# Kernel tuning notes

Hardware: AMD Instinct MI355X
Metric: run time of the kernel (lower is better)

Reference implementation:

```python
import jax, jax.numpy as jnp
import numpy as np

H = W = 9
C = 16
D = 34
NHEAD = 2
HDIM = D // NHEAD  # 17
FF = 2048
NLAYERS = 2
EPS = 1e-5


def setup_inputs() -> dict:
    key = jax.random.key(0)
    ks = jax.random.split(key, 16)
    s = 0.05
    return {
        "obs": jax.random.normal(ks[0], (2, H, W), dtype=jnp.float32),
        "conv1_w": jax.random.normal(ks[1], (16, 2, 3, 3), dtype=jnp.float32) * s,
        "conv1_b": jnp.zeros((16,), jnp.float32),
        "conv2_w": jax.random.normal(ks[2], (16, 16, 3, 3), dtype=jnp.float32) * s,
        "conv2_b": jnp.zeros((16,), jnp.float32),
        "in_proj_w": jax.random.normal(ks[3], (NLAYERS, 3 * D, D), dtype=jnp.float32) * s,
        "in_proj_b": jnp.zeros((NLAYERS, 3 * D), jnp.float32),
        "out_proj_w": jax.random.normal(ks[4], (NLAYERS, D, D), dtype=jnp.float32) * s,
        "out_proj_b": jnp.zeros((NLAYERS, D), jnp.float32),
        "lin1_w": jax.random.normal(ks[5], (NLAYERS, FF, D), dtype=jnp.float32) * s,
        "lin1_b": jnp.zeros((NLAYERS, FF), jnp.float32),
        "lin2_w": jax.random.normal(ks[6], (NLAYERS, D, FF), dtype=jnp.float32) * s,
        "lin2_b": jnp.zeros((NLAYERS, D), jnp.float32),
        "ln1_g": jnp.ones((NLAYERS, D), jnp.float32),
        "ln1_b": jnp.zeros((NLAYERS, D), jnp.float32),
        "ln2_g": jnp.ones((NLAYERS, D), jnp.float32),
        "ln2_b": jnp.zeros((NLAYERS, D), jnp.float32),
    }


def _layer_norm(x, g, b):
    m = jnp.mean(x, axis=-1, keepdims=True)
    v = jnp.mean(jnp.square(x - m), axis=-1, keepdims=True)
    return (x - m) * jax.lax.rsqrt(v + EPS) * g + b


def _encoder_layer(x, ipw, ipb, opw, opb, l1w, l1b, l2w, l2b, g1, b1, g2, b2):
    # x: [S, D]. Post-norm TransformerEncoderLayer, eval mode (no dropout).
    S = x.shape[0]
    qkv = x @ ipw.T + ipb  # [S, 3D]
    q, k, v = jnp.split(qkv, 3, axis=-1)
    q = q.reshape(S, NHEAD, HDIM).transpose(1, 0, 2)  # [h, S, d]
    k = k.reshape(S, NHEAD, HDIM).transpose(1, 0, 2)
    v = v.reshape(S, NHEAD, HDIM).transpose(1, 0, 2)
    scores = jnp.einsum("hqd,hkd->hqk", q, k) / jnp.sqrt(jnp.float32(HDIM))
    attn = jax.nn.softmax(scores, axis=-1)
    o = jnp.einsum("hqk,hkd->hqd", attn, v)  # [h, S, d]
    o = o.transpose(1, 0, 2).reshape(S, D)
    o = o @ opw.T + opb
    x = _layer_norm(x + o, g1, b1)
    f = jax.nn.relu(x @ l1w.T + l1b) @ l2w.T + l2b
    return _layer_norm(x + f, g2, b2)


def _conv(x, w, b):
    y = jax.lax.conv_general_dilated(
        x, w, window_strides=(1, 1), padding="SAME",
        dimension_numbers=("NCHW", "OIHW", "NCHW"))
    return jax.nn.relu(y + b[None, :, None, None])


def reference(obs, conv1_w, conv1_b, conv2_w, conv2_b, in_proj_w, in_proj_b,
              out_proj_w, out_proj_b, lin1_w, lin1_b, lin2_w, lin2_b,
              ln1_g, ln1_b, ln2_g, ln2_b):
    x = obs[None]  # [1, 2, H, W]
    x = _conv(x, conv1_w, conv1_b)
    x = _conv(x, conv2_w, conv2_b)
    hw = H * W
    cell_emb = x[0].reshape(C, hw).T  # [hw, C]
    idx = jnp.arange(hw)
    r = (idx // W).astype(jnp.float32)
    c = (idx % W).astype(jnp.float32)
    dx = (r[:, None] - r[None, :]) / ((H - 1) / 2.0)  # [hw, hw]
    dy = (c[:, None] - c[None, :]) / ((W - 1) / 2.0)
    tok_i = jnp.broadcast_to(cell_emb[:, None, :], (hw, hw, C))
    tok_j = jnp.broadcast_to(cell_emb[None, :, :], (hw, hw, C))
    rel = jnp.stack([dx, dy], axis=-1)  # [hw, hw, 2]
    tokens = jnp.concatenate([tok_i, tok_j, rel], axis=-1).reshape(hw * hw, D)
    for l in range(NLAYERS):
        tokens = _encoder_layer(
            tokens, in_proj_w[l], in_proj_b[l], out_proj_w[l], out_proj_b[l],
            lin1_w[l], lin1_b[l], lin2_w[l], lin2_b[l],
            ln1_g[l], ln1_b[l], ln2_g[l], ln2_b[l])
    agent_idx = jnp.argmax(obs[0].reshape(-1))
    start = agent_idx * hw
    agent_tokens = jax.lax.dynamic_slice(tokens, (start, 0), (hw, D))
    return agent_tokens.mean(axis=0)  # [D]
```

## Files before the change

### kernel.cpp

```cpp
#include <hip/hip_runtime.h>
#include <hip/hip_bf16.h>

#define HH 9
#define WW 9
#define HW 81
#define CC 16
#define DD 34
#define SS 6561
#define NHEAD 2
#define HD 17
#define FF 2048
#define EPSF 1e-5f

#define NTILES 52
#define NSPLIT2 26
#define QB 64

#define NIP 7168
#define NOP 3072
#define NW1 131072
#define NW2 98304
#define NLTOT (NIP + NOP + NW1 + NW2)
#define LPREP_BLOCKS 1872
#define NKF 425984
#define NVF 212992
#define NV16 13312
#define ZERO_WORDS 332800
#define ZERO_BLOCKS 1300

#define NEAB 124416
#define NVFL1 12288

typedef __attribute__((ext_vector_type(8))) short bf16x8;
typedef __attribute__((ext_vector_type(4))) float f32x4;

__device__ __forceinline__ unsigned short f2b(float f) {
  unsigned int u = __float_as_uint(f);
  u += 0x7fffu + ((u >> 16) & 1u);
  return (unsigned short)(u >> 16);
}

__global__ __launch_bounds__(256) void prep_kernel(
    const float* __restrict__ obs, const float* __restrict__ w1, const float* __restrict__ b1,
    const float* __restrict__ w2, const float* __restrict__ b2,
    float* __restrict__ cell, int* __restrict__ aidx,
    const float* __restrict__ ipw, const float* __restrict__ opw,
    const float* __restrict__ l1w, const float* __restrict__ l2w,
    unsigned short* __restrict__ ipwp, unsigned short* __restrict__ opwp,
    unsigned short* __restrict__ w1p, unsigned short* __restrict__ w2p,
    unsigned short* __restrict__ kfp, unsigned short* __restrict__ vfp,
    float* __restrict__ v16) {
  int bx = blockIdx.x;
  int t = threadIdx.x;
  if (bx == 0) {
    __shared__ float s_obs[2][11][11];
    __shared__ float s_w1[288];
    __shared__ float s_w2[2304];
    __shared__ float s_b1[16], s_b2[16];
    __shared__ float y1[CC][121];
    for (int i = t; i < 2 * 121; i += 256) ((float*)s_obs)[i] = 0.f;
    for (int i = t; i < CC * 121; i += 256) ((float*)y1)[i] = 0.f;
    for (int i = t; i < 288; i += 256) s_w1[i] = w1[i];
    for (int i = t; i < 2304; i += 256) s_w2[i] = w2[i];
    if (t < 16) { s_b1[t] = b1[t]; s_b2[t] = b2[t]; }
    __syncthreads();
    for (int i = t; i < 2 * HW; i += 256) {
      int ic = i / HW, p = i % HW;
      s_obs[ic][1 + p / WW][1 + p % WW] = obs[i];
    }
    __syncthreads();
    if (t == 0) {
      int best = 0; float bv = s_obs[0][1][1];
      for (int p = 1; p < HW; p++) {
        float v = s_obs[0][1 + p / WW][1 + p % WW];
        if (v > bv) { bv = v; best = p; }
      }
      *aidx = best;
    }
    for (int idx = t; idx < CC * HW; idx += 256) {
      int c = idx / HW, p = idx % HW;
      int i = p / WW, j = p % WW;
      float acc = s_b1[c];
#pragma unroll
      for (int ic = 0; ic < 2; ic++)
#pragma unroll
        for (int di = 0; di < 3; di++)
#pragma unroll
          for (int dj = 0; dj < 3; dj++)
            acc += s_obs[ic][i + di][j + dj] * s_w1[((c * 2 + ic) * 3 + di) * 3 + dj];
      y1[c][(i + 1) * 11 + (j + 1)] = fmaxf(acc, 0.f);
    }
    __syncthreads();
    for (int idx = t; idx < CC * HW; idx += 256) {
      int c = idx / HW, p = idx % HW;
      int i = p / WW, j = p % WW;
      float acc = s_b2[c];
#pragma unroll
      for (int ic = 0; ic < CC; ic++)
#pragma unroll
        for (int di = 0; di < 3; di++)
#pragma unroll
          for (int dj = 0; dj < 3; dj++)
            acc += y1[ic][(i + di) * 11 + (j + dj)] * s_w2[((c * CC + ic) * 3 + di) * 3 + dj];
      cell[p * CC + c] = fmaxf(acc, 0.f);
    }
  } else if (bx <= LPREP_BLOCKS) {
    int i = (bx - 1) * 256 + t;
    int layer = i / NLTOT;
    int r = i % NLTOT;
    if (r < NIP) {
      int n = r >> 6, k = r & 63;
      ipwp[layer * NIP + r] =
          (n < 102 && k < DD) ? f2b(ipw[(size_t)layer * 102 * DD + n * DD + k]) : (unsigned short)0;
    } else if (r < NIP + NOP) {
      int rr = r - NIP;
      int n = rr >> 6, k = rr & 63;
      opwp[layer * NOP + rr] =
          (n < DD && k < DD) ? f2b(opw[(size_t)layer * DD * DD + n * DD + k]) : (unsigned short)0;
    } else if (r < NIP + NOP + NW1) {
      int rr = r - NIP - NOP;
      int f = rr >> 6, k = rr & 63;
      w1p[layer * NW1 + rr] =
          (k < DD) ? f2b(l1w[(size_t)layer * FF * DD + f * DD + k]) : (unsigned short)0;
    } else {
      int rr = r - NIP - NOP - NW1;
      int d = rr >> 11, kk = rr & 2047;
      w2p[layer * NW2 + rr] =
          (d < DD) ? f2b(l2w[(size_t)layer * DD * FF + d * FF + kk]) : (unsigned short)0;
    }
  } else {
    int zi = (bx - 1 - LPREP_BLOCKS) * 256 + t;
    if (zi < NKF / 2) ((unsigned int*)kfp)[zi] = 0u;
    else if (zi < NKF / 2 + NVF / 2) ((unsigned int*)vfp)[zi - NKF / 2] = 0u;
    else if (zi < ZERO_WORDS) v16[zi - NKF / 2 - NVF / 2] = 0.f;
  }
}

__global__ __launch_bounds__(256) void ptprep_kernel(
    const float* __restrict__ cell, const float* __restrict__ ipw,
    const float* __restrict__ ipb, float* __restrict__ Pt) {
  int idx = blockIdx.x * 256 + threadIdx.x;
  if (idx >= 2 * HW * 102) return;
  int part = idx / (HW * 102);
  int rem = idx % (HW * 102);
  int a = rem / 102, n = rem % 102;
  float ra = (float)(a / WW) * 0.25f, ca = (float)(a % WW) * 0.25f;
  float acc;
  if (part == 0) {
    acc = ipb[n] + ipw[n * DD + 32] * ra + ipw[n * DD + 33] * ca;
    for (int f = 0; f < CC; f++) acc += ipw[n * DD + f] * cell[a * CC + f];
  } else {
    acc = -(ipw[n * DD + 32] * ra + ipw[n * DD + 33] * ca);
    for (int f = 0; f < CC; f++) acc += ipw[n * DD + CC + f] * cell[a * CC + f];
  }
  Pt[idx] = acc;
}

__global__ __launch_bounds__(256) void expprep_kernel(
    const float* __restrict__ Pt, float* __restrict__ eAB,
    unsigned short* __restrict__ vfragL1) {
  int idx = blockIdx.x * 256 + threadIdx.x;
  const float scale = 0.24253562503633297f;
  if (idx < NEAB) {
    int a = idx % 96; int rest = idx / 96;
    int row = rest % 81; rest /= 81;
    int ab = rest & 1, p = (rest >> 1) & 1, h = rest >> 2;
    float e = 0.f;
    if (a < HW) {
      const float* qrow = Pt + (size_t)ab * (HW * 102) + row * 102 + h * HD;
      const float* krow = Pt + (size_t)p * (HW * 102) + a * 102 + DD + h * HD;
      float dot = 0.f;
#pragma unroll
      for (int d = 0; d < HD; d++) dot += qrow[d] * krow[d];
      e = __expf(fminf(dot * scale, 40.f));
    }
    eAB[idx] = e;
  } else if (idx < NEAB + NVFL1) {
    int j = idx - NEAB;
    int a = j % 96; int rest = j / 96;
    int n = rest % 32; rest /= 32;
    int p = rest & 1, h = rest >> 1;
    float v = 0.f;
    if (a < HW) {
      if (n < HD) v = Pt[(size_t)p * (HW * 102) + a * 102 + 2 * DD + h * HD + n];
      else if (n == HD) v = 1.f;
    }
    vfragL1[((size_t)(h * 2 + p) * 32 + n) * 96 + a] = f2b(v);
  }
}

__global__ __launch_bounds__(256) void fl1_kernel(
    const float* __restrict__ cell, const float* __restrict__ eAB,
    const unsigned short* __restrict__ vfragL1,
    const unsigned short* __restrict__ opwp, const float* __restrict__ opb,
    const float* __restrict__ g1v, const float* __restrict__ b1v,
    const unsigned short* __restrict__ w1p, const unsigned short* __restrict__ w2p,
    const float* __restrict__ fb1, const float* __restrict__ fb2,
    const float* __restrict__ g2v, const float* __restrict__ b2v,
    float* __restrict__ x) {
  __shared__ __align__(16) unsigned short sE[4][16 * 96];
  __shared__ __align__(16) unsigned short soA[16 * 72];
  __shared__ float sxF[16][35];
  __shared__ __align__(16) unsigned short sxA2[16 * 72];
  __shared__ float sxF2[16][35];
  __shared__ __align__(16) unsigned short hw_[4][16 * 40];
  __shared__ float yred[4][16][49];
  int t = threadIdx.x;
  int w = t >> 6, lane = t & 63, quad = lane >> 4, col = lane & 15;
  int r0 = blockIdx.x * 16;
  int nr = min(16, SS - r0);

  for (int i = t; i < 16 * 72; i += 256) { soA[i] = 0; sxA2[i] = 0; }
  for (int i = t; i < 16 * 35; i += 256) { ((float*)sxF)[i] = 0.f; ((float*)sxF2)[i] = 0.f; }
  for (int i = t; i < nr * DD; i += 256) {
    int r = i / DD, d = i - r * DD;
    int row = r0 + r;
    int ii = row / HW, jj = row - ii * HW;
    float v;
    if (d < CC) v = cell[ii * CC + d];
    else if (d < 2 * CC) v = cell[jj * CC + (d - CC)];
    else if (d == 32) v = (float)((ii / WW) - (jj / WW)) * 0.25f;
    else v = (float)((ii % WW) - (jj % WW)) * 0.25f;
    sxF[r][d] = v;
  }

  {
    int h = w >> 1, p = w & 1;
    const float* eA = eAB + ((size_t)((h * 2 + p) * 2 + 0) * 81) * 96;
    const float* eB = eAB + ((size_t)((h * 2 + p) * 2 + 1) * 81) * 96;
    int tl = lane >> 2, asub = lane & 3;
    int row = r0 + tl;
    int tc = row < SS ? row : SS - 1;
    int it = tc / HW, jt = tc - it * HW;
    const float* eAr = eA + it * 96 + asub * 24;
    const float* eBr = eB + jt * 96 + asub * 24;
    unsigned short etmp[24];
#pragma unroll
    for (int k = 0; k < 24; k++) etmp[k] = f2b(eAr[k] * eBr[k]);
    unsigned short* Eb = &sE[w][tl * 96 + asub * 24];
#pragma unroll
    for (int k = 0; k < 3; k++)
      *(bf16x8*)(Eb + k * 8) = *(bf16x8*)(etmp + k * 8);
    const unsigned short* vf = vfragL1 + (size_t)(h * 2 + p) * 32 * 96;
    f32x4 acc0 = {0.f, 0.f, 0.f, 0.f}, acc1 = {0.f, 0.f, 0.f, 0.f};
#pragma unroll
    for (int c = 0; c < 3; c++) {
      bf16x8 ea = *(const bf16x8*)&sE[w][col * 96 + c * 32 + quad * 8];
      bf16x8 vb0 = *(const bf16x8*)&vf[col * 96 + c * 32 + quad * 8];
      bf16x8 vb1 = *(const bf16x8*)&vf[(16 + col) * 96 + c * 32 + quad * 8];
      acc0 = __builtin_amdgcn_mfma_f32_16x16x32_bf16(ea, vb0, acc0, 0, 0, 0);
      acc1 = __builtin_amdgcn_mfma_f32_16x16x32_bf16(ea, vb1, acc1, 0, 0, 0);
    }
    float Sr[4];
#pragma unroll
    for (int r = 0; r < 4; r++) Sr[r] = __shfl(acc1[r], (lane & 48) + 1);
#pragma unroll
    for (int r = 0; r < 4; r++) {
      int rr = quad * 4 + r;
      float inv = 1.f / Sr[r];
      yred[w][rr][col] = acc0[r] * inv;
      if (col == 0) yred[w][rr][16] = acc1[r] * inv;
    }
  }
  __syncthreads();
  for (int i = t; i < 16 * DD; i += 256) {
    int r = i / DD, dd = i - r * DD;
    int h2 = dd / HD, d2 = dd - h2 * HD;
    soA[r * 72 + dd] = f2b(yred[2 * h2][r][d2] + yred[2 * h2 + 1][r][d2]);
  }
  __syncthreads();

  if (w == 0) {
    bf16x8 a0 = *(const bf16x8*)&soA[col * 72 + quad * 8];
    bf16x8 a1 = *(const bf16x8*)&soA[col * 72 + 32 + quad * 8];
    f32x4 y[3];
#pragma unroll
    for (int nt = 0; nt < 3; nt++) {
      int n = nt * 16 + col;
      bf16x8 b0 = *(const bf16x8*)&opwp[n * 64 + quad * 8];
      bf16x8 b1 = *(const bf16x8*)&opwp[n * 64 + 32 + quad * 8];
      f32x4 acc = {0.f, 0.f, 0.f, 0.f};
      acc = __builtin_amdgcn_mfma_f32_16x16x32_bf16(a0, b0, acc, 0, 0, 0);
      y[nt] = __builtin_amdgcn_mfma_f32_16x16x32_bf16(a1, b1, acc, 0, 0, 0);
    }
    float yv[3][4];
    float s1[4] = {0.f, 0.f, 0.f, 0.f}, s2[4] = {0.f, 0.f, 0.f, 0.f};
#pragma unroll
    for (int nt = 0; nt < 3; nt++) {
      int d = nt * 16 + col;
      bool vd = d < DD;
      float ob = vd ? opb[d] : 0.f;
#pragma unroll
      for (int r = 0; r < 4; r++) {
        int row = quad * 4 + r;
        float v = vd ? (y[nt][r] + ob + sxF[row][d]) : 0.f;
        yv[nt][r] = v;
        s1[r] += v;
        s2[r] += v * v;
      }
    }
#pragma unroll
    for (int msk = 1; msk <= 8; msk <<= 1)
#pragma unroll
      for (int r = 0; r < 4; r++) {
        s1[r] += __shfl_xor(s1[r], msk);
        s2[r] += __shfl_xor(s2[r], msk);
      }
#pragma unroll
    for (int r = 0; r < 4; r++) {
      int row = quad * 4 + r;
      float mean = s1[r] * (1.f / DD);
      float var = s2[r] * (1.f / DD) - mean * mean;
      float rs = rsqrtf(var + EPSF);
#pragma unroll
      for (int nt = 0; nt < 3; nt++) {
        int d = nt * 16 + col;
        if (d < DD) {
          float o = (yv[nt][r] - mean) * rs * g1v[d] + b1v[d];
          sxF2[row][d] = o;
          sxA2[row * 72 + d] = f2b(o);
        }
      }
    }
  }
  __syncthreads();

  bf16x8 a0 = *(const bf16x8*)&sxA2[col * 72 + quad * 8];
  bf16x8 a1 = *(const bf16x8*)&sxA2[col * 72 + 32 + quad * 8];
  unsigned short* myh = &hw_[w][0];
  f32x4 acc3[3];
#pragma unroll
  for (int nt = 0; nt < 3; nt++) acc3[nt] = (f32x4){0.f, 0.f, 0.f, 0.f};
  for (int kt = 0; kt < 16; kt++) {
    int fbase = kt * 128 + w * 32;
#pragma unroll
    for (int nt = 0; nt < 2; nt++) {
      int f = fbase + nt * 16 + col;
      bf16x8 b0f = *(const bf16x8*)&w1p[f * 64 + quad * 8];
      bf16x8 b1f = *(const bf16x8*)&w1p[f * 64 + 32 + quad * 8];
      f32x4 hacc = {0.f, 0.f, 0.f, 0.f};
      hacc = __builtin_amdgcn_mfma_f32_16x16x32_bf16(a0, b0f, hacc, 0, 0, 0);
      hacc = __builtin_amdgcn_mfma_f32_16x16x32_bf16(a1, b1f, hacc, 0, 0, 0);
      float bias = fb1[f];
#pragma unroll
      for (int r = 0; r < 4; r++) {
        float hv = fmaxf(hacc[r] + bias, 0.f);
        myh[(quad * 4 + r) * 40 + nt * 16 + col] = f2b(hv);
      }
    }
    bf16x8 pa = *(const bf16x8*)&myh[col * 40 + quad * 8];
#pragma unroll
    for (int nt = 0; nt < 3; nt++) {
      int n = nt * 16 + col;
      bf16x8 wb = *(const bf16x8*)&w2p[(size_t)n * FF + fbase + quad * 8];
      acc3[nt] = __builtin_amdgcn_mfma_f32_16x16x32_bf16(pa, wb, acc3[nt], 0, 0, 0);
    }
  }
#pragma unroll
  for (int nt = 0; nt < 3; nt++)
#pragma unroll
    for (int r = 0; r < 4; r++)
      yred[w][quad * 4 + r][nt * 16 + col] = acc3[nt][r];
  __syncthreads();
  if (w == 0) {
    float yv[3][4];
    float s1[4] = {0.f, 0.f, 0.f, 0.f}, s2[4] = {0.f, 0.f, 0.f, 0.f};
#pragma unroll
    for (int nt = 0; nt < 3; nt++) {
      int d = nt * 16 + col;
      bool valid = d < DD;
      float b2x = valid ? fb2[d] : 0.f;
#pragma unroll
      for (int r = 0; r < 4; r++) {
        int row = quad * 4 + r;
        float v = yred[0][row][nt * 16 + col] + yred[1][row][nt * 16 + col]
                + yred[2][row][nt * 16 + col] + yred[3][row][nt * 16 + col];
        v = valid ? (v + b2x + sxF2[row][d]) : 0.f;
        yv[nt][r] = v;
        s1[r] += v;
        s2[r] += v * v;
      }
    }
#pragma unroll
    for (int msk = 1; msk <= 8; msk <<= 1)
#pragma unroll
      for (int r = 0; r < 4; r++) {
        s1[r] += __shfl_xor(s1[r], msk);
        s2[r] += __shfl_xor(s2[r], msk);
      }
#pragma unroll
    for (int r = 0; r < 4; r++) {
      int row = quad * 4 + r;
      if (row >= nr) continue;
      float mean = s1[r] * (1.f / DD);
      float var = s2[r] * (1.f / DD) - mean * mean;
      float rs = rsqrtf(var + EPSF);
#pragma unroll
      for (int nt = 0; nt < 3; nt++) {
        int d = nt * 16 + col;
        if (d < DD)
          x[(size_t)(r0 + row) * DD + d] = (yv[nt][r] - mean) * rs * g2v[d] + b2v[d];
      }
    }
  }
}

__global__ __launch_bounds__(256) void qkv2_kernel(
    const float* __restrict__ x, const unsigned short* __restrict__ ipwp,
    const float* __restrict__ ipb, const int* __restrict__ abase,
    float* __restrict__ qkv, unsigned short* __restrict__ kfp,
    unsigned short* __restrict__ vfp, float* __restrict__ v16) {
  __shared__ __align__(16) unsigned short sxA[32 * 72];
  int t = threadIdx.x;
  int w = t >> 6, lane = t & 63, quad = lane >> 4, col = lane & 15;
  int m0 = (w & 1) * 16, half = w >> 1;
  bool qpart = blockIdx.x >= 206;
  int row0 = qpart ? (abase[0] * HW + (blockIdx.x - 206) * 32) : blockIdx.x * 32;
  int nr = min(32, SS - row0);
  for (int i = t; i < 32 * 72; i += 256) sxA[i] = 0;
  __syncthreads();
  for (int i = t; i < nr * DD; i += 256) {
    int r = i / DD, d = i - r * DD;
    sxA[r * 72 + d] = f2b(x[(size_t)(row0 + r) * DD + d]);
  }
  __syncthreads();
  bf16x8 a0 = *(const bf16x8*)&sxA[(m0 + col) * 72 + quad * 8];
  bf16x8 a1 = *(const bf16x8*)&sxA[(m0 + col) * 72 + 32 + quad * 8];
  if (!qpart) {
    int ntc = half ? 2 : 3;
    for (int nt2 = 0; nt2 < ntc; nt2++) {
      int nt = half * 3 + nt2;
      int n = DD + nt * 16 + col;
      int nc = n < 112 ? n : 111;
      bf16x8 b0 = *(const bf16x8*)&ipwp[nc * 64 + quad * 8];
      bf16x8 b1 = *(const bf16x8*)&ipwp[nc * 64 + 32 + quad * 8];
      f32x4 acc = {0.f, 0.f, 0.f, 0.f};
      acc = __builtin_amdgcn_mfma_f32_16x16x32_bf16(a0, b0, acc, 0, 0, 0);
      acc = __builtin_amdgcn_mfma_f32_16x16x32_bf16(a1, b1, acc, 0, 0, 0);
      if (n < 102) {
        float bias = ipb[n];
        int kd = n - DD;
#pragma unroll
        for (int r = 0; r < 4; r++) {
          int m = m0 + quad * 4 + r;
          if (m >= nr) continue;
          int tok = row0 + m;
          float val = acc[r] + bias;
          int T = tok >> 7, tl = tok & 127;
          if (kd < 2 * HD) {
            int h = kd >= HD;
            int d = kd - h * HD;
            int colf = tl >> 3, ntk = tl & 7;
            kfp[(((size_t)h * NTILES + T) * 8 + ntk) * 512 +
                ((d >> 3) * 16 + colf) * 8 + (d & 7)] = f2b(val);
          } else {
            int vd = kd - 2 * HD;
            int h = vd >= HD;
            int d = vd - h * HD;
            if (d < 16) {
              int c = tl >> 5, qf = (tl >> 3) & 3, j = tl & 7;
              vfp[(((size_t)h * NTILES + T) * 4 + c) * 512 +
                  (qf * 16 + d) * 8 + j] = f2b(val);
            } else {
              v16[(size_t)h * (NTILES * 128) + tok] = val;
            }
          }
        }
      }
    }
  } else {
    int ntc = half ? 1 : 2;
    for (int nt2 = 0; nt2 < ntc; nt2++) {
      int nt = half * 2 + nt2;
      int n = nt * 16 + col;
      bf16x8 b0 = *(const bf16x8*)&ipwp[n * 64 + quad * 8];
      bf16x8 b1 = *(const bf16x8*)&ipwp[n * 64 + 32 + quad * 8];
      f32x4 acc = {0.f, 0.f, 0.f, 0.f};
      acc = __builtin_amdgcn_mfma_f32_16x16x32_bf16(a0, b0, acc, 0, 0, 0);
      acc = __builtin_amdgcn_mfma_f32_16x16x32_bf16(a1, b1, acc, 0, 0, 0);
      if (n < DD) {
        float bias = ipb[n];
#pragma unroll
        for (int r = 0; r < 4; r++) {
          int m = row0 + m0 + quad * 4 + r;
          if (m < SS) qkv[(size_t)m * 102 + n] = acc[r] + bias;
        }
      }
    }
  }
}

__global__ __launch_bounds__(256) void attn2_kernel(
    const float* __restrict__ qkv, const unsigned short* __restrict__ kfp,
    const unsigned short* __restrict__ vfp, const float* __restrict__ v16,
    const int* __restrict__ abase,
    float* __restrict__ opart, float* __restrict__ lpart) {
  __shared__ __align__(16) unsigned short scb[4][16 * 136];
  int t = threadIdx.x, w = t >> 6, lane = t & 63, quad = lane >> 4, col = lane & 15;
  int h = blockIdx.y, sp = blockIdx.z;
  int base = abase[0] * HW;
  int q0 = blockIdx.x * QB;
  const float scale = 0.24253562503633297f;
  const unsigned short* kf = kfp + (size_t)h * (NTILES * 8 * 512);
  const unsigned short* vf = vfp + (size_t)h * (NTILES * 4 * 512);
  const float* v16h = v16 + (size_t)h * (NTILES * 128);
  unsigned short* myscb = &scb[w][0];

  int mq = base + q0 + w * 16 + col;
  int qc = mq < SS ? mq : SS - 1;
  bf16x8 aq;
#pragma unroll
  for (int j = 0; j < 8; j++) {
    int d = quad * 8 + j;
    aq[j] = (short)((d < HD) ? f2b(qkv[(size_t)qc * 102 + h * HD + d] * scale) : 0);
  }

  f32x4 oacc = {0.f, 0.f, 0.f, 0.f};
  float o16a[4] = {0.f, 0.f, 0.f, 0.f};
  float lreg[4] = {0.f, 0.f, 0.f, 0.f};

  for (int tile = sp; tile < NTILES; tile += NSPLIT2) {
    int k0 = tile * 128;
    const unsigned short* kt = kf + (size_t)tile * (8 * 512);
    f32x4 s[8];
#pragma unroll
    for (int nt = 0; nt < 8; nt++) {
      bf16x8 kb = *(const bf16x8*)(kt + nt * 512 + lane * 8);
      f32x4 z = {0.f, 0.f, 0.f, 0.f};
      s[nt] = __builtin_amdgcn_mfma_f32_16x16x32_bf16(aq, kb, z, 0, 0, 0);
    }
    if (k0 + 128 > SS) {
#pragma unroll
      for (int nt = 0; nt < 8; nt++)
        if (k0 + col * 8 + nt >= SS) {
          s[nt][0] = -1e30f; s[nt][1] = -1e30f; s[nt][2] = -1e30f; s[nt][3] = -1e30f;
        }
    }
#pragma unroll
    for (int r = 0; r < 4; r++) {
      bf16x8 pv;
      float psl = 0.f;
#pragma unroll
      for (int nt = 0; nt < 8; nt++) {
        float p = __expf(fminf(s[nt][r], 70.f));
        s[nt][r] = p;
        psl += p;
        pv[nt] = (short)f2b(p);
      }
      lreg[r] += psl;
      *(bf16x8*)(myscb + (quad * 4 + r) * 136 + col * 8) = pv;
    }
    f32x4 va = *(const f32x4*)(v16h + k0 + col * 8);
    f32x4 vb4 = *(const f32x4*)(v16h + k0 + col * 8 + 4);
#pragma unroll
    for (int r = 0; r < 4; r++) {
      o16a[r] += s[0][r] * va[0] + s[1][r] * va[1] + s[2][r] * va[2] + s[3][r] * va[3]
               + s[4][r] * vb4[0] + s[5][r] * vb4[1] + s[6][r] * vb4[2] + s[7][r] * vb4[3];
    }
    const unsigned short* vt = vf + (size_t)tile * (4 * 512);
#pragma unroll
    for (int c = 0; c < 4; c++) {
      bf16x8 pa = *(const bf16x8*)(myscb + col * 136 + c * 32 + quad * 8);
      bf16x8 vbf = *(const bf16x8*)(vt + c * 512 + lane * 8);
      oacc = __builtin_amdgcn_mfma_f32_16x16x32_bf16(pa, vbf, oacc, 0, 0, 0);
    }
  }
#pragma unroll
  for (int msk = 1; msk <= 8; msk <<= 1)
#pragma unroll
    for (int r = 0; r < 4; r++) {
      o16a[r] += __shfl_xor(o16a[r], msk);
      lreg[r] += __shfl_xor(lreg[r], msk);
    }
  size_t obase = ((size_t)sp * NHEAD + h) * 128;
#pragma unroll
  for (int r = 0; r < 4; r++) {
    int ql = q0 + w * 16 + quad * 4 + r;
    if (ql < HW) {
      opart[(obase + ql) * HD + col] = oacc[r];
      if (col == 0) {
        opart[(obase + ql) * HD + 16] = o16a[r];
        lpart[obase + ql] = lreg[r];
      }
    }
  }
}

__global__ __launch_bounds__(256) void fl2_kernel(
    const float* __restrict__ opart, const float* __restrict__ lpart,
    const unsigned short* __restrict__ opwp, const float* __restrict__ opb,
    const float* __restrict__ g1v, const float* __restrict__ b1v,
    const unsigned short* __restrict__ w1p, const unsigned short* __restrict__ w2p,
    const float* __restrict__ fb1, const float* __restrict__ fb2,
    const float* __restrict__ g2v, const float* __restrict__ b2v,
    const int* __restrict__ abase, float* __restrict__ x) {
  __shared__ __align__(16) unsigned short soA[16 * 72];
  __shared__ float sxF[16][35];
  __shared__ __align__(16) unsigned short sxA2[16 * 72];
  __shared__ float sxF2[16][35];
  __shared__ __align__(16) unsigned short hw_[4][16 * 40];
  __shared__ float yred[4][16][49];
  int t = threadIdx.x;
  int w = t >> 6, lane = t & 63, quad = lane >> 4, col = lane & 15;
  int base = abase[0] * HW;
  int ql0 = blockIdx.x * 16;
  int nr = min(16, HW - ql0);
  int r0 = base + ql0;

  for (int i = t; i < 16 * 72; i += 256) { soA[i] = 0; sxA2[i] = 0; }
  for (int i = t; i < 16 * 35; i += 256) { ((float*)sxF)[i] = 0.f; ((float*)sxF2)[i] = 0.f; }
  __syncthreads();
  for (int i = t; i < nr * DD; i += 256) {
    int r = i / DD, rem = i - r * DD;
    sxF[r][rem] = x[(size_t)(r0 + r) * DD + rem];
    int ql = ql0 + r;
    int h = rem / HD, d = rem - h * HD;
    float L = 0.f, O = 0.f;
#pragma unroll
    for (int s = 0; s < NSPLIT2; s++) {
      L += lpart[((size_t)s * NHEAD + h) * 128 + ql];
      O += opart[(((size_t)s * NHEAD + h) * 128 + ql) * HD + d];
    }
    soA[r * 72 + rem] = f2b(O / L);
  }
  __syncthreads();
  if (w == 0) {
    bf16x8 a0 = *(const bf16x8*)&soA[col * 72 + quad * 8];
    bf16x8 a1 = *(const bf16x8*)&soA[col * 72 + 32 + quad * 8];
    f32x4 y[3];
#pragma unroll
    for (int nt = 0; nt < 3; nt++) {
      int n = nt * 16 + col;
      bf16x8 b0 = *(const bf16x8*)&opwp[n * 64 + quad * 8];
      bf16x8 b1 = *(const bf16x8*)&opwp[n * 64 + 32 + quad * 8];
      f32x4 acc = {0.f, 0.f, 0.f, 0.f};
      acc = __builtin_amdgcn_mfma_f32_16x16x32_bf16(a0, b0, acc, 0, 0, 0);
      y[nt] = __builtin_amdgcn_mfma_f32_16x16x32_bf16(a1, b1, acc, 0, 0, 0);
    }
    float yv[3][4];
    float s1[4] = {0.f, 0.f, 0.f, 0.f}, s2[4] = {0.f, 0.f, 0.f, 0.f};
#pragma unroll
    for (int nt = 0; nt < 3; nt++) {
      int d = nt * 16 + col;
      bool vd = d < DD;
      float ob = vd ? opb[d] : 0.f;
#pragma unroll
      for (int r = 0; r < 4; r++) {
        int row = quad * 4 + r;
        float v = vd ? (y[nt][r] + ob + sxF[row][d]) : 0.f;
        yv[nt][r] = v;
        s1[r] += v;
        s2[r] += v * v;
      }
    }
#pragma unroll
    for (int msk = 1; msk <= 8; msk <<= 1)
#pragma unroll
      for (int r = 0; r < 4; r++) {
        s1[r] += __shfl_xor(s1[r], msk);
        s2[r] += __shfl_xor(s2[r], msk);
      }
#pragma unroll
    for (int r = 0; r < 4; r++) {
      int row = quad * 4 + r;
      float mean = s1[r] * (1.f / DD);
      float var = s2[r] * (1.f / DD) - mean * mean;
      float rs = rsqrtf(var + EPSF);
#pragma unroll
      for (int nt = 0; nt < 3; nt++) {
        int d = nt * 16 + col;
        if (d < DD) {
          float o = (yv[nt][r] - mean) * rs * g1v[d] + b1v[d];
          sxF2[row][d] = o;
          sxA2[row * 72 + d] = f2b(o);
        }
      }
    }
  }
  __syncthreads();
  bf16x8 a0 = *(const bf16x8*)&sxA2[col * 72 + quad * 8];
  bf16x8 a1 = *(const bf16x8*)&sxA2[col * 72 + 32 + quad * 8];
  unsigned short* myh = &hw_[w][0];
  f32x4 acc3[3];
#pragma unroll
  for (int nt = 0; nt < 3; nt++) acc3[nt] = (f32x4){0.f, 0.f, 0.f, 0.f};
  for (int kt = 0; kt < 16; kt++) {
    int fbase = kt * 128 + w * 32;
#pragma unroll
    for (int nt = 0; nt < 2; nt++) {
      int f = fbase + nt * 16 + col;
      bf16x8 b0f = *(const bf16x8*)&w1p[f * 64 + quad * 8];
      bf16x8 b1f = *(const bf16x8*)&w1p[f * 64 + 32 + quad * 8];
      f32x4 hacc = {0.f, 0.f, 0.f, 0.f};
      hacc = __builtin_amdgcn_mfma_f32_16x16x32_bf16(a0, b0f, hacc, 0, 0, 0);
      hacc = __builtin_amdgcn_mfma_f32_16x16x32_bf16(a1, b1f, hacc, 0, 0, 0);
      float bias = fb1[f];
#pragma unroll
      for (int r = 0; r < 4; r++) {
        float hv = fmaxf(hacc[r] + bias, 0.f);
        myh[(quad * 4 + r) * 40 + nt * 16 + col] = f2b(hv);
      }
    }
    bf16x8 pa = *(const bf16x8*)&myh[col * 40 + quad * 8];
#pragma unroll
    for (int nt = 0; nt < 3; nt++) {
      int n = nt * 16 + col;
      bf16x8 wb = *(const bf16x8*)&w2p[(size_t)n * FF + fbase + quad * 8];
      acc3[nt] = __builtin_amdgcn_mfma_f32_16x16x32_bf16(pa, wb, acc3[nt], 0, 0, 0);
    }
  }
#pragma unroll
  for (int nt = 0; nt < 3; nt++)
#pragma unroll
    for (int r = 0; r < 4; r++)
      yred[w][quad * 4 + r][nt * 16 + col] = acc3[nt][r];
  __syncthreads();
  if (w == 0) {
    float yv[3][4];
    float s1[4] = {0.f, 0.f, 0.f, 0.f}, s2[4] = {0.f, 0.f, 0.f, 0.f};
#pragma unroll
    for (int nt = 0; nt < 3; nt++) {
      int d = nt * 16 + col;
      bool valid = d < DD;
      float b2x = valid ? fb2[d] : 0.f;
#pragma unroll
      for (int r = 0; r < 4; r++) {
        int row = quad * 4 + r;
        float v = yred[0][row][nt * 16 + col] + yred[1][row][nt * 16 + col]
                + yred[2][row][nt * 16 + col] + yred[3][row][nt * 16 + col];
        v = valid ? (v + b2x + sxF2[row][d]) : 0.f;
        yv[nt][r] = v;
        s1[r] += v;
        s2[r] += v * v;
      }
    }
#pragma unroll
    for (int msk = 1; msk <= 8; msk <<= 1)
#pragma unroll
      for (int r = 0; r < 4; r++) {
        s1[r] += __shfl_xor(s1[r], msk);
        s2[r] += __shfl_xor(s2[r], msk);
      }
#pragma unroll
    for (int r = 0; r < 4; r++) {
      int row = quad * 4 + r;
      if (row >= nr) continue;
      float mean = s1[r] * (1.f / DD);
      float var = s2[r] * (1.f / DD) - mean * mean;
      float rs = rsqrtf(var + EPSF);
#pragma unroll
      for (int nt = 0; nt < 3; nt++) {
        int d = nt * 16 + col;
        if (d < DD)
          x[(size_t)(r0 + row) * DD + d] = (yv[nt][r] - mean) * rs * g2v[d] + b2v[d];
      }
    }
  }
}

__global__ __launch_bounds__(64) void final_kernel(
    const float* __restrict__ x, const int* __restrict__ aidx, float* __restrict__ out) {
  int d = threadIdx.x;
  if (d >= DD) return;
  int start = (*aidx) * HW;
  float acc = 0.f;
  for (int j = 0; j < HW; j++) acc += x[(size_t)(start + j) * DD + d];
  out[d] = acc * (1.f / HW);
}

extern "C" void kernel_launch(void* const* d_in, const int* in_sizes, int n_in,
                              void* d_out, int out_size, void* d_ws, size_t ws_size,
                              hipStream_t stream) {
  const float* obs = (const float*)d_in[0];
  const float* c1w = (const float*)d_in[1];
  const float* c1b = (const float*)d_in[2];
  const float* c2w = (const float*)d_in[3];
  const float* c2b = (const float*)d_in[4];
  const float* ipw = (const float*)d_in[5];
  const float* ipb = (const float*)d_in[6];
  const float* opw = (const float*)d_in[7];
  const float* opb = (const float*)d_in[8];
  const float* l1w = (const float*)d_in[9];
  const float* l1b = (const float*)d_in[10];
  const float* l2w = (const float*)d_in[11];
  const float* l2b = (const float*)d_in[12];
  const float* g1 = (const float*)d_in[13];
  const float* b1 = (const float*)d_in[14];
  const float* g2 = (const float*)d_in[15];
  const float* b2 = (const float*)d_in[16];
  float* out = (float*)d_out;

  float* ws = (float*)d_ws;
  size_t off = 0;
  float* x     = ws + off; off += SS * DD;
  float* qkv   = ws + off; off += SS * 102;
  float* cell  = ws + off; off += HW * CC;
  int*   aidx  = (int*)(ws + off); off += 1;
  off = (off + 3) & ~(size_t)3;
  float* Pt    = ws + off; off += 2 * HW * 102;
  float* opart = ws + off; off += (size_t)NSPLIT2 * NHEAD * 128 * HD;
  float* lpart = ws + off; off += (size_t)NSPLIT2 * NHEAD * 128;
  float* eAB   = ws + off; off += NEAB;
  off = (off + 3) & ~(size_t)3;
  unsigned short* vfragL1 = (unsigned short*)(ws + off); off += NVFL1 / 2;
  unsigned short* kfp  = (unsigned short*)(ws + off); off += NKF / 2;
  unsigned short* vfp  = (unsigned short*)(ws + off); off += NVF / 2;
  float* v16 = ws + off; off += NV16;
  unsigned short* ipwp = (unsigned short*)(ws + off); off += 2 * NIP / 2;
  unsigned short* opwp = (unsigned short*)(ws + off); off += 2 * NOP / 2;
  unsigned short* w1p  = (unsigned short*)(ws + off); off += 2 * NW1 / 2;
  unsigned short* w2p  = (unsigned short*)(ws + off); off += 2 * NW2 / 2;

  const int prep_grid = 1 + LPREP_BLOCKS + ZERO_BLOCKS;
  const int pt_blocks = (2 * HW * 102 + 255) / 256;
  const int exp_blocks = (NEAB + NVFL1 + 255) / 256;
  const int fl1_blocks = (SS + 15) / 16;

  prep_kernel<<<prep_grid, 256, 0, stream>>>(
      obs, c1w, c1b, c2w, c2b, cell, aidx,
      ipw, opw, l1w, l2w, ipwp, opwp, w1p, w2p, kfp, vfp, v16);
  ptprep_kernel<<<pt_blocks, 256, 0, stream>>>(cell, ipw, ipb, Pt);
  expprep_kernel<<<exp_blocks, 256, 0, stream>>>(Pt, eAB, vfragL1);
  fl1_kernel<<<fl1_blocks, 256, 0, stream>>>(
      cell, eAB, vfragL1, opwp, opb, g1, b1, w1p, w2p, l1b, l2b, g2, b2, x);
  qkv2_kernel<<<210, 256, 0, stream>>>(
      x, ipwp + NIP, ipb + 102, aidx, qkv, kfp, vfp, v16);
  dim3 a2g(2, NHEAD, NSPLIT2);
  attn2_kernel<<<a2g, 256, 0, stream>>>(qkv, kfp, vfp, v16, aidx, opart, lpart);
  fl2_kernel<<<6, 256, 0, stream>>>(
      opart, lpart, opwp + NOP, opb + DD, g1 + DD, b1 + DD,
      w1p + NW1, w2p + NW2, l1b + FF, l2b + DD, g2 + DD, b2 + DD, aidx, x);
  final_kernel<<<1, 64, 0, stream>>>(x, aidx, out);
}
```

Baseline: 195.5 us.

## Split layer-2 FFN over the hidden dimension across blocks with a reduction kernel

The final-layer FFN kernel previously ran on only 6 blocks, each looping over all 2048 hidden units. It now splits the hidden dimension into 8 chunks across a second grid axis, giving 48 blocks. Each block writes partial FFN outputs to workspace, and a new small kernel sums the partials, adds the bias and residual, and applies the second LayerNorm. This trades one extra launch, partial-sum traffic and redundant attention-output/LN1 recomputation per split for more parallelism on a latency-bound tail stage.

```diff
diff --git a/kernel.cpp b/kernel.cpp
--- a/kernel.cpp
+++ b/kernel.cpp
@@ -30,6 +30,7 @@
 
 #define NEAB 124416
 #define NVFL1 12288
+#define KSPLIT 8
 
 typedef __attribute__((ext_vector_type(8))) short bf16x8;
 typedef __attribute__((ext_vector_type(4))) float f32x4;
@@ -586,14 +587,13 @@
   }
 }
 
-__global__ __launch_bounds__(256) void fl2_kernel(
+__global__ __launch_bounds__(256) void fl2a_kernel(
     const float* __restrict__ opart, const float* __restrict__ lpart,
     const unsigned short* __restrict__ opwp, const float* __restrict__ opb,
     const float* __restrict__ g1v, const float* __restrict__ b1v,
     const unsigned short* __restrict__ w1p, const unsigned short* __restrict__ w2p,
-    const float* __restrict__ fb1, const float* __restrict__ fb2,
-    const float* __restrict__ g2v, const float* __restrict__ b2v,
-    const int* __restrict__ abase, float* __restrict__ x) {
+    const float* __restrict__ fb1, const int* __restrict__ abase,
+    const float* __restrict__ x, float* __restrict__ xln, float* __restrict__ ypart) {
   __shared__ __align__(16) unsigned short soA[16 * 72];
   __shared__ float sxF[16][35];
   __shared__ __align__(16) unsigned short sxA2[16 * 72];
@@ -602,6 +602,7 @@
   __shared__ float yred[4][16][49];
   int t = threadIdx.x;
   int w = t >> 6, lane = t & 63, quad = lane >> 4, col = lane & 15;
+  int sp = blockIdx.y;
   int base = abase[0] * HW;
   int ql0 = blockIdx.x * 16;
   int nr = min(16, HW - ql0);
@@ -673,6 +674,8 @@
           float o = (yv[nt][r] - mean) * rs * g1v[d] + b1v[d];
           sxF2[row][d] = o;
           sxA2[row * 72 + d] = f2b(o);
+          if (sp == 0 && row < nr)
+            xln[(size_t)(ql0 + row) * DD + d] = o;
         }
       }
     }
@@ -684,7 +687,8 @@
   f32x4 acc3[3];
 #pragma unroll
   for (int nt = 0; nt < 3; nt++) acc3[nt] = (f32x4){0.f, 0.f, 0.f, 0.f};
-  for (int kt = 0; kt < 16; kt++) {
+  for (int kt2 = 0; kt2 < 2; kt2++) {
+    int kt = sp * 2 + kt2;
     int fbase = kt * 128 + w * 32;
 #pragma unroll
     for (int nt = 0; nt < 2; nt++) {
@@ -716,46 +720,45 @@
       yred[w][quad * 4 + r][nt * 16 + col] = acc3[nt][r];
   __syncthreads();
   if (w == 0) {
-    float yv[3][4];
-    float s1[4] = {0.f, 0.f, 0.f, 0.f}, s2[4] = {0.f, 0.f, 0.f, 0.f};
-#pragma unroll
-    for (int nt = 0; nt < 3; nt++) {
-      int d = nt * 16 + col;
-      bool valid = d < DD;
-      float b2x = valid ? fb2[d] : 0.f;
-#pragma unroll
-      for (int r = 0; r < 4; r++) {
-        int row = quad * 4 + r;
-        float v = yred[0][row][nt * 16 + col] + yred[1][row][nt * 16 + col]
-                + yred[2][row][nt * 16 + col] + yred[3][row][nt * 16 + col];
-        v = valid ? (v + b2x + sxF2[row][d]) : 0.f;
-        yv[nt][r] = v;
-        s1[r] += v;
-        s2[r] += v * v;
-      }
-    }
-#pragma unroll
-    for (int msk = 1; msk <= 8; msk <<= 1)
-#pragma unroll
-      for (int r = 0; r < 4; r++) {
-        s1[r] += __shfl_xor(s1[r], msk);
-        s2[r] += __shfl_xor(s2[r], msk);
-      }
-#pragma unroll
-    for (int r = 0; r < 4; r++) {
-      int row = quad * 4 + r;
-      if (row >= nr) continue;
-      float mean = s1[r] * (1.f / DD);
-      float var = s2[r] * (1.f / DD) - mean * mean;
-      float rs = rsqrtf(var + EPSF);
-#pragma unroll
-      for (int nt = 0; nt < 3; nt++) {
-        int d = nt * 16 + col;
-        if (d < DD)
-          x[(size_t)(r0 + row) * DD + d] = (yv[nt][r] - mean) * rs * g2v[d] + b2v[d];
-      }
-    }
-  }
+    for (int i = lane; i < nr * DD; i += 64) {
+      int r = i / DD, d = i - r * DD;
+      float v = yred[0][r][d] + yred[1][r][d] + yred[2][r][d] + yred[3][r][d];
+      ypart[((size_t)sp * HW + ql0 + r) * DD + d] = v;
+    }
+  }
+}
+
+__global__ __launch_bounds__(256) void fl2b_kernel(
+    const float* __restrict__ ypart, const float* __restrict__ xln,
+    const float* __restrict__ fb2, const float* __restrict__ g2v,
+    const float* __restrict__ b2v, const int* __restrict__ abase,
+    float* __restrict__ x) {
+  int t = threadIdx.x;
+  int row = blockIdx.x * 32 + (t >> 3);
+  int s8 = t & 7;
+  if (row >= HW) return;
+  int base = abase[0] * HW;
+  float yv[5];
+  float s1 = 0.f, s2 = 0.f;
+  int cnt = 0;
+  for (int d = s8; d < DD; d += 8) {
+    float v = fb2[d] + xln[(size_t)row * DD + d];
+#pragma unroll
+    for (int sp = 0; sp < KSPLIT; sp++)
+      v += ypart[((size_t)sp * HW + row) * DD + d];
+    yv[cnt++] = v;
+    s1 += v;
+    s2 += v * v;
+  }
+  s1 += __shfl_xor(s1, 1); s2 += __shfl_xor(s2, 1);
+  s1 += __shfl_xor(s1, 2); s2 += __shfl_xor(s2, 2);
+  s1 += __shfl_xor(s1, 4); s2 += __shfl_xor(s2, 4);
+  float mean = s1 * (1.f / DD);
+  float var = s2 * (1.f / DD) - mean * mean;
+  float rs = rsqrtf(var + EPSF);
+  cnt = 0;
+  for (int d = s8; d < DD; d += 8)
+    x[(size_t)(base + row) * DD + d] = (yv[cnt++] - mean) * rs * g2v[d] + b2v[d];
 }
 
 __global__ __launch_bounds__(64) void final_kernel(
@@ -801,6 +804,8 @@
   float* opart = ws + off; off += (size_t)NSPLIT2 * NHEAD * 128 * HD;
   float* lpart = ws + off; off += (size_t)NSPLIT2 * NHEAD * 128;
   float* eAB   = ws + off; off += NEAB;
+  float* xln   = ws + off; off += HW * DD;
+  float* ypart = ws + off; off += (size_t)KSPLIT * HW * DD;
   off = (off + 3) & ~(size_t)3;
   unsigned short* vfragL1 = (unsigned short*)(ws + off); off += NVFL1 / 2;
   unsigned short* kfp  = (unsigned short*)(ws + off); off += NKF / 2;
@@ -827,8 +832,11 @@
       x, ipwp + NIP, ipb + 102, aidx, qkv, kfp, vfp, v16);
   dim3 a2g(2, NHEAD, NSPLIT2);
   attn2_kernel<<<a2g, 256, 0, stream>>>(qkv, kfp, vfp, v16, aidx, opart, lpart);
-  fl2_kernel<<<6, 256, 0, stream>>>(
+  dim3 f2g(6, KSPLIT);
+  fl2a_kernel<<<f2g, 256, 0, stream>>>(
       opart, lpart, opwp + NOP, opb + DD, g1 + DD, b1 + DD,
-      w1p + NW1, w2p + NW2, l1b + FF, l2b + DD, g2 + DD, b2 + DD, aidx, x);
+      w1p + NW1, w2p + NW2, l1b + FF, aidx, x, xln, ypart);
+  fl2b_kernel<<<3, 256, 0, stream>>>(
+      ypart, xln, l2b + DD, g2 + DD, b2 + DD, aidx, x);
   final_kernel<<<1, 64, 0, stream>>>(x, aidx, out);
 }
```

Result: faster. 187.5 us (-4.1%).
